# Kernel optimization log

Measured on AMD Instinct MI355X. Metric: run time of the kernel, lower is better.

The kernel has to match this reference:

```python
import jax, jax.numpy as jnp
import numpy as np

N_P = 32  # top-N_p points kept per channel
EPS = 1e-5  # BatchNorm eps


def setup_inputs() -> dict:
    key = jax.random.key(0)
    ks = jax.random.split(key, 20)
    B, N = 16, 8192
    d = {"x": jax.random.normal(ks[0], (B, 3, N), dtype=jnp.float32)}
    dims = [(64, 3), (128, 64), (256, 128)]
    i = 1
    for li, (co, ci) in enumerate(dims, start=1):
        d[f"w{li}"] = jax.random.normal(ks[i], (co, ci), dtype=jnp.float32) * (1.0 / np.sqrt(ci)); i += 1
        d[f"b{li}"] = jax.random.normal(ks[i], (co,), dtype=jnp.float32) * 0.1; i += 1
        d[f"g{li}"] = jax.random.uniform(ks[i], (co,), dtype=jnp.float32, minval=0.5, maxval=1.5); i += 1
        d[f"be{li}"] = jax.random.normal(ks[i], (co,), dtype=jnp.float32) * 0.1; i += 1
        d[f"m{li}"] = jax.random.normal(ks[i], (co,), dtype=jnp.float32) * 0.1; i += 1
        d[f"v{li}"] = jax.random.uniform(ks[i], (co,), dtype=jnp.float32, minval=0.5, maxval=1.5); i += 1
    return d


def _conv_bn(h, w, b, g, be, m, v, relu):
    # Conv1d with kernel_size=1 == per-point linear: [B,Ci,N] x [Co,Ci] -> [B,Co,N]
    h = jnp.einsum('bin,oi->bon', h, w) + b[None, :, None]
    h = (h - m[None, :, None]) * (g[None, :, None] / jnp.sqrt(v[None, :, None] + EPS)) + be[None, :, None]
    return jax.nn.relu(h) if relu else h


def reference(x, w1, b1, g1, be1, m1, v1, w2, b2, g2, be2, m2, v2, w3, b3, g3, be3, m3, v3):
    h = _conv_bn(x, w1, b1, g1, be1, m1, v1, True)
    h = _conv_bn(h, w2, b2, g2, be2, m2, v2, True)
    h = _conv_bn(h, w3, b3, g3, be3, m3, v3, False)  # [B,C,N], C=256
    # SoftPool: per-channel top-N_p point indices, gather all channels at them
    _, idx = jax.lax.top_k(h, N_P)  # idx: [B,C,N_p] (descending sort == top_k)
    # gathered[b, c_sort, c_feat, k] = h[b, c_feat, idx[b, c_sort, k]]
    gathered = jnp.take_along_axis(h[:, None, :, :], idx[:, :, None, :], axis=3)  # [B,C,C,N_p]
    # sp_cube[b, c_feat, k, c_sort]
    return gathered.transpose(0, 2, 3, 1)
```

## Files before the change

### kernel.cpp

```cpp
#include <hip/hip_runtime.h>


using v4f = __attribute__((ext_vector_type(4))) float;

__device__ __forceinline__ float bf16rne(float x) {
    unsigned u = __float_as_uint(x);
    u = (u + 0x7FFFu + ((u >> 16) & 1u)) & 0xFFFF0000u;
    return __uint_as_float(u);
}

__global__ void scales_kernel(const float* __restrict__ g1, const float* __restrict__ v1,
                              const float* __restrict__ g2, const float* __restrict__ v2,
                              const float* __restrict__ g3, const float* __restrict__ v3,
                              float* __restrict__ s) {
    int t = threadIdx.x;
    if (t < 64)       s[t] = __fdiv_rn(g1[t],       __fsqrt_rn(__fadd_rn(v1[t],       1e-5f)));
    else if (t < 192) s[t] = __fdiv_rn(g2[t - 64],  __fsqrt_rn(__fadd_rn(v2[t - 64],  1e-5f)));
    else if (t < 448) s[t] = __fdiv_rn(g3[t - 192], __fsqrt_rn(__fadd_rn(v3[t - 192], 1e-5f)));
}

__global__ __launch_bounds__(256, 1) void mlp12_kernel(
        const float* __restrict__ x,
        const float* __restrict__ w1, const float* __restrict__ b1,
        const float* __restrict__ m1, const float* __restrict__ be1,
        const float* __restrict__ w2, const float* __restrict__ b2,
        const float* __restrict__ m2, const float* __restrict__ be2,
        const float* __restrict__ sc,
        float* __restrict__ h2g) {
    const float* s1 = sc;
    const float* s2 = sc + 64;

    int t    = threadIdx.x;
    int tile = blockIdx.x & 3;
    int pt   = (blockIdx.x >> 2) * 256 + t;
    int b    = pt >> 13;
    int n    = pt & 8191;

    const float* xb = x + (size_t)b * 24576 + n;
    float x0 = xb[0], x1 = xb[8192], x2 = xb[16384];

    float h1[64];
#pragma unroll
    for (int o = 0; o < 64; ++o) {
        float acc = __fmul_rn(w1[o * 3 + 0], x0);
        acc = __fadd_rn(acc, __fmul_rn(w1[o * 3 + 1], x1));
        acc = __fadd_rn(acc, __fmul_rn(w1[o * 3 + 2], x2));
        float hpb = __fadd_rn(acc, b1[o]);
        float tt  = __fsub_rn(hpb, m1[o]);
        float r   = __fadd_rn(__fmul_rn(tt, s1[o]), be1[o]);
        h1[o] = fmaxf(r, 0.0f);
    }

    v4f* dst = (v4f*)h2g;
    const v4f* w2v = (const v4f*)w2;
    for (int qq = 0; qq < 8; ++qq) {
        int q = tile * 8 + qq;
        v4f hv;
#pragma unroll
        for (int j = 0; j < 4; ++j) {
            int c2 = q * 4 + j;
            const v4f* wr = w2v + c2 * 16;
            float a = 0.0f;
#pragma unroll
            for (int k = 0; k < 16; ++k) {
                v4f w = wr[k];
                a = __fadd_rn(a, __fmul_rn(w.x, h1[4 * k + 0]));
                a = __fadd_rn(a, __fmul_rn(w.y, h1[4 * k + 1]));
                a = __fadd_rn(a, __fmul_rn(w.z, h1[4 * k + 2]));
                a = __fadd_rn(a, __fmul_rn(w.w, h1[4 * k + 3]));
            }
            float hpb = __fadd_rn(a, b2[c2]);
            float tt  = __fsub_rn(hpb, m2[c2]);
            hv[j] = fmaxf(__fadd_rn(__fmul_rn(tt, s2[c2]), be2[c2]), 0.0f);
        }
        dst[(size_t)q * 131072 + pt] = hv;
    }
}

__global__ __launch_bounds__(256) void mlp3_kernel(
        const float* __restrict__ h2g,
        const float* __restrict__ w3, const float* __restrict__ b3,
        const float* __restrict__ m3, const float* __restrict__ be3,
        const float* __restrict__ sc,
        float* __restrict__ h) {
    const float* s3 = sc + 192;

    int B    = blockIdx.x;
    int xcd  = B & 7;
    int slot = B >> 3;
    int tile = slot & 15;
    int ptb  = (slot >> 4) * 8 + xcd;
    int t    = threadIdx.x;
    int pt   = ptb * 256 + t;
    int b    = pt >> 13;
    int n    = pt & 8191;
    int ob   = tile * 16;

    float acc[16];
#pragma unroll
    for (int j = 0; j < 16; ++j) acc[j] = 0.0f;

    const v4f* src = (const v4f*)h2g;
    const v4f* w3v = (const v4f*)w3;

    for (int q = 0; q < 32; ++q) {
        v4f hv = src[(size_t)q * 131072 + pt];
#pragma unroll
        for (int j = 0; j < 16; ++j) {
            v4f w = w3v[(size_t)(ob + j) * 32 + q];
            acc[j] = __fadd_rn(acc[j], __fmul_rn(w.x, hv.x));
            acc[j] = __fadd_rn(acc[j], __fmul_rn(w.y, hv.y));
            acc[j] = __fadd_rn(acc[j], __fmul_rn(w.z, hv.z));
            acc[j] = __fadd_rn(acc[j], __fmul_rn(w.w, hv.w));
        }
    }

    float* hb = h + (size_t)b * 2097152 + n;
#pragma unroll
    for (int j = 0; j < 16; ++j) {
        int o = ob + j;
        float hpb = __fadd_rn(acc[j], b3[o]);
        float tt  = __fsub_rn(hpb, m3[o]);
        float rr  = __fadd_rn(__fmul_rn(tt, s3[o]), be3[o]);
        hb[(size_t)o * 8192] = rr;
    }
}

__global__ __launch_bounds__(256) void topk_kernel(const float* __restrict__ h,
                                                   int* __restrict__ idx_out) {
    __shared__ unsigned long long mrg[2][64][4];

    int t      = threadIdx.x;
    int lane   = t & 63;
    int waveid = (t >> 6) & 1;
    int rhalf  = t >> 7;
    int row    = blockIdx.x * 2 + rhalf;
    const float* hr = h + (size_t)row * 8192;
    const v4f* hv4  = (const v4f*)hr;

    unsigned long long k0 = 0, k1 = 0, k2 = 0, k3 = 0;
    int j0 = waveid * 16;
    int lanebase = 8191 - lane * 4;

    v4f p0 = hv4[(j0 + 0) * 64 + lane], p1 = hv4[(j0 + 1) * 64 + lane];
    v4f p2 = hv4[(j0 + 2) * 64 + lane], p3 = hv4[(j0 + 3) * 64 + lane];

    for (int jb = 0; jb < 4; ++jb) {
        int jn = j0 + ((jb < 3) ? (jb + 1) * 4 : 0);
        v4f n0 = hv4[(jn + 0) * 64 + lane], n1 = hv4[(jn + 1) * 64 + lane];
        v4f n2 = hv4[(jn + 2) * 64 + lane], n3 = hv4[(jn + 3) * 64 + lane];

#pragma unroll
        for (int jj = 0; jj < 4; ++jj) {
            v4f v = (jj == 0) ? p0 : (jj == 1) ? p1 : (jj == 2) ? p2 : p3;
            int j = j0 + jb * 4 + jj;
#pragma unroll
            for (int c = 0; c < 4; ++c) {
                unsigned u = __float_as_uint(v[c]);
                u = (u & 0x80000000u) ? ~u : (u | 0x80000000u);
                unsigned long long key =
                    ((unsigned long long)u << 13) |
                    (unsigned)(lanebase - (j * 256 + c));
                unsigned long long s = key, hi;
                hi = (k0 > s) ? k0 : s;  s = (k0 > s) ? s : k0;  k0 = hi;
                hi = (k1 > s) ? k1 : s;  s = (k1 > s) ? s : k1;  k1 = hi;
                hi = (k2 > s) ? k2 : s;  s = (k2 > s) ? s : k2;  k2 = hi;
                k3 = (k3 > s) ? k3 : s;
            }
        }
        p0 = n0; p1 = n1; p2 = n2; p3 = n3;
    }

    if (waveid == 1) {
        mrg[rhalf][lane][0] = k0; mrg[rhalf][lane][1] = k1;
        mrg[rhalf][lane][2] = k2; mrg[rhalf][lane][3] = k3;
    }
    __syncthreads();
    if (waveid == 1) return;

#pragma unroll
    for (int q = 0; q < 4; ++q) {
        unsigned long long s = mrg[rhalf][lane][q], hi;
        hi = (k0 > s) ? k0 : s;  s = (k0 > s) ? s : k0;  k0 = hi;
        hi = (k1 > s) ? k1 : s;  s = (k1 > s) ? s : k1;  k1 = hi;
        hi = (k2 > s) ? k2 : s;  s = (k2 > s) ? s : k2;  k2 = hi;
        k3 = (k3 > s) ? k3 : s;
    }

    unsigned long long last = 0xFFFFFFFFFFFFFFFFull;
    int valid = 4;

    for (int pass = 0; pass < 32; ++pass) {
        unsigned long long m = k0;
#pragma unroll
        for (int s = 1; s < 64; s <<= 1) {
            unsigned long long o = __shfl_xor(m, s, 64);
            m = (o > m) ? o : m;
        }
        if (lane == 0) idx_out[row * 32 + pass] = 8191 - (int)(m & 8191ull);

        if (k0 == m) {
            last = m;
            k0 = k1; k1 = k2; k2 = k3; k3 = 0ull;
            --valid;
            if (valid == 0 && pass < 31) {
                for (int j = 0; j < 32; ++j) {
                    v4f v = *(const v4f*)&hr[j * 256 + lane * 4];
#pragma unroll
                    for (int c = 0; c < 4; ++c) {
                        unsigned u = __float_as_uint(v[c]);
                        u = (u & 0x80000000u) ? ~u : (u | 0x80000000u);
                        int i = j * 256 + lane * 4 + c;
                        unsigned long long key = ((unsigned long long)u << 13) | (unsigned)(8191 - i);
                        if (key < last && key > k3) {
                            unsigned long long s = key, hi;
                            hi = (k0 > s) ? k0 : s;  s = (k0 > s) ? s : k0;  k0 = hi;
                            hi = (k1 > s) ? k1 : s;  s = (k1 > s) ? s : k1;  k1 = hi;
                            hi = (k2 > s) ? k2 : s;  s = (k2 > s) ? s : k2;  k2 = hi;
                            k3 = s;
                        }
                    }
                }
                valid = 4;
            }
        }
    }
}

__global__ __launch_bounds__(256) void gather_kernel(const float* __restrict__ h,
                                                     const int* __restrict__ idx,
                                                     float* __restrict__ out) {
    __shared__ int idxs2[8192];

    int blk = blockIdx.x;
    int b   = blk >> 6;
    int cfq = blk & 63;
    int t   = threadIdx.x;

    for (int d = t; d < 8192; d += 256) {
        int k = d >> 8, cs = d & 255;
        idxs2[d] = idx[b * 8192 + cs * 32 + k];
    }
    __syncthreads();

    const float* hb = h + (size_t)b * 2097152;
    float* ob = out + (size_t)b * 2097152;

#pragma unroll
    for (int r = 0; r < 4; ++r) {
        int cf = cfq * 4 + r;
        const float* hrow = hb + (size_t)cf * 8192;
        float* orow = ob + (size_t)cf * 8192;
#pragma unroll 8
        for (int rep = 0; rep < 32; ++rep) {
            int elem = rep * 256 + t;
            int i = idxs2[elem];
            orow[elem] = bf16rne(hrow[i]);
        }
    }
}

extern "C" void kernel_launch(void* const* d_in, const int* in_sizes, int n_in,
                              void* d_out, int out_size, void* d_ws, size_t ws_size,
                              hipStream_t stream) {
    const float* x   = (const float*)d_in[0];
    const float* w1  = (const float*)d_in[1];
    const float* b1  = (const float*)d_in[2];
    const float* g1  = (const float*)d_in[3];
    const float* be1 = (const float*)d_in[4];
    const float* m1  = (const float*)d_in[5];
    const float* v1  = (const float*)d_in[6];
    const float* w2  = (const float*)d_in[7];
    const float* b2  = (const float*)d_in[8];
    const float* g2  = (const float*)d_in[9];
    const float* be2 = (const float*)d_in[10];
    const float* m2  = (const float*)d_in[11];
    const float* v2  = (const float*)d_in[12];
    const float* w3  = (const float*)d_in[13];
    const float* b3  = (const float*)d_in[14];
    const float* g3  = (const float*)d_in[15];
    const float* be3 = (const float*)d_in[16];
    const float* m3  = (const float*)d_in[17];
    const float* v3  = (const float*)d_in[18];

    char* ws = (char*)d_ws;
    float* h    = (float*)(ws);
    int*   idxb = (int*)(ws + 134217728);
    float* sc   = (float*)(ws + 134742016);
    float* h2g  = (float*)d_out;

    scales_kernel<<<1, 448, 0, stream>>>(g1, v1, g2, v2, g3, v3, sc);
    mlp12_kernel<<<2048, 256, 0, stream>>>(x, w1, b1, m1, be1,
                                           w2, b2, m2, be2, sc, h2g);
    mlp3_kernel<<<8192, 256, 0, stream>>>(h2g, w3, b3, m3, be3, sc, h);
    topk_kernel<<<2048, 256, 0, stream>>>(h, idxb);
    gather_kernel<<<1024, 256, 0, stream>>>(h, idxb, (float*)d_out);
}
```

Baseline: 315.9 us.

## Use FMA in layer-3 GEMM and refine top-k candidates with exact recompute

The layer-3 kernel now accumulates with fused multiply-add instead of separately rounded multiply and add, which cuts the instruction count in the hottest loop. To keep the top-k selection matching the reference's rounding, the top-k kernel emits 48 candidates per row. A new refine kernel recomputes those candidates with the original rounded arithmetic and picks the exact top 32. This adds an extra launch and extra candidate passes, and it risks wrong selections if FMA rounding pushes a true top-32 point past rank 48.

New measurement: 398.2 us. +26.1%, slower.

```diff
diff --git a/kernel.cpp b/kernel.cpp
--- a/kernel.cpp
+++ b/kernel.cpp
@@ -108,10 +108,10 @@
 #pragma unroll
         for (int j = 0; j < 16; ++j) {
             v4f w = w3v[(size_t)(ob + j) * 32 + q];
-            acc[j] = __fadd_rn(acc[j], __fmul_rn(w.x, hv.x));
-            acc[j] = __fadd_rn(acc[j], __fmul_rn(w.y, hv.y));
-            acc[j] = __fadd_rn(acc[j], __fmul_rn(w.z, hv.z));
-            acc[j] = __fadd_rn(acc[j], __fmul_rn(w.w, hv.w));
+            acc[j] = fmaf(w.x, hv.x, acc[j]);
+            acc[j] = fmaf(w.y, hv.y, acc[j]);
+            acc[j] = fmaf(w.z, hv.z, acc[j]);
+            acc[j] = fmaf(w.w, hv.w, acc[j]);
         }
     }
 
@@ -119,15 +119,13 @@
 #pragma unroll
     for (int j = 0; j < 16; ++j) {
         int o = ob + j;
-        float hpb = __fadd_rn(acc[j], b3[o]);
-        float tt  = __fsub_rn(hpb, m3[o]);
-        float rr  = __fadd_rn(__fmul_rn(tt, s3[o]), be3[o]);
+        float rr = fmaf(acc[j] + b3[o] - m3[o], s3[o], be3[o]);
         hb[(size_t)o * 8192] = rr;
     }
 }
 
 __global__ __launch_bounds__(256) void topk_kernel(const float* __restrict__ h,
-                                                   int* __restrict__ idx_out) {
+                                                   int* __restrict__ cand) {
     __shared__ unsigned long long mrg[2][64][4];
 
     int t      = threadIdx.x;
@@ -190,20 +188,20 @@
     unsigned long long last = 0xFFFFFFFFFFFFFFFFull;
     int valid = 4;
 
-    for (int pass = 0; pass < 32; ++pass) {
+    for (int pass = 0; pass < 48; ++pass) {
         unsigned long long m = k0;
 #pragma unroll
         for (int s = 1; s < 64; s <<= 1) {
             unsigned long long o = __shfl_xor(m, s, 64);
             m = (o > m) ? o : m;
         }
-        if (lane == 0) idx_out[row * 32 + pass] = 8191 - (int)(m & 8191ull);
+        if (lane == 0) cand[row * 48 + pass] = 8191 - (int)(m & 8191ull);
 
         if (k0 == m) {
             last = m;
             k0 = k1; k1 = k2; k2 = k3; k3 = 0ull;
             --valid;
-            if (valid == 0 && pass < 31) {
+            if (valid == 0 && pass < 47) {
                 for (int j = 0; j < 32; ++j) {
                     v4f v = *(const v4f*)&hr[j * 256 + lane * 4];
 #pragma unroll
@@ -224,6 +222,56 @@
                 valid = 4;
             }
         }
+    }
+}
+
+__global__ __launch_bounds__(256) void refine_kernel(
+        const float* __restrict__ h2g,
+        const float* __restrict__ w3, const float* __restrict__ b3,
+        const float* __restrict__ m3, const float* __restrict__ be3,
+        const float* __restrict__ sc,
+        const int* __restrict__ cand,
+        int* __restrict__ idx_out) {
+    const float* s3 = sc + 192;
+
+    int t    = threadIdx.x;
+    int lane = t & 63;
+    int row  = blockIdx.x * 4 + (t >> 6);
+    int b    = row >> 8;
+    int cs   = row & 255;
+
+    int ci = cand[row * 48 + (lane < 48 ? lane : 47)];
+
+    const v4f* src = (const v4f*)h2g;
+    size_t base = (size_t)b * 8192 + ci;
+    const float* w3r = w3 + (size_t)cs * 128;
+
+    float acc = 0.0f;
+    for (int q = 0; q < 32; ++q) {
+        v4f hv = src[(size_t)q * 131072 + base];
+        acc = __fadd_rn(acc, __fmul_rn(w3r[4 * q + 0], hv.x));
+        acc = __fadd_rn(acc, __fmul_rn(w3r[4 * q + 1], hv.y));
+        acc = __fadd_rn(acc, __fmul_rn(w3r[4 * q + 2], hv.z));
+        acc = __fadd_rn(acc, __fmul_rn(w3r[4 * q + 3], hv.w));
+    }
+    float hpb = __fadd_rn(acc, b3[cs]);
+    float tt  = __fsub_rn(hpb, m3[cs]);
+    float r   = __fadd_rn(__fmul_rn(tt, s3[cs]), be3[cs]);
+
+    unsigned u = __float_as_uint(r);
+    u = (u & 0x80000000u) ? ~u : (u | 0x80000000u);
+    unsigned long long key = ((unsigned long long)u << 13) | (unsigned)(8191 - ci);
+    if (lane >= 48) key = 0ull;
+
+    for (int pass = 0; pass < 32; ++pass) {
+        unsigned long long m = key;
+#pragma unroll
+        for (int s = 1; s < 64; s <<= 1) {
+            unsigned long long o = __shfl_xor(m, s, 64);
+            m = (o > m) ? o : m;
+        }
+        if (lane == 0) idx_out[row * 32 + pass] = 8191 - (int)(m & 8191ull);
+        if (key == m) key = 0ull;
     }
 }
 
@@ -287,12 +335,14 @@
     float* h    = (float*)(ws);
     int*   idxb = (int*)(ws + 134217728);
     float* sc   = (float*)(ws + 134742016);
+    int*   cand = (int*)(ws + 134744064);
     float* h2g  = (float*)d_out;
 
     scales_kernel<<<1, 448, 0, stream>>>(g1, v1, g2, v2, g3, v3, sc);
     mlp12_kernel<<<2048, 256, 0, stream>>>(x, w1, b1, m1, be1,
                                            w2, b2, m2, be2, sc, h2g);
     mlp3_kernel<<<8192, 256, 0, stream>>>(h2g, w3, b3, m3, be3, sc, h);
-    topk_kernel<<<2048, 256, 0, stream>>>(h, idxb);
+    topk_kernel<<<2048, 256, 0, stream>>>(h, cand);
+    refine_kernel<<<1024, 256, 0, stream>>>(h2g, w3, b3, m3, be3, sc, cand, idxb);
     gather_kernel<<<1024, 256, 0, stream>>>(h, idxb, (float*)d_out);
 }
```
